# Optimization experiments

Hardware: AMD Instinct MI355X
Metric: run time of the kernel (lower is better)

## Reference

```python
import jax, jax.numpy as jnp
import numpy as np

NUM_HEADS = 16


def setup_inputs() -> dict:
    key = jax.random.key(0)
    ks = jax.random.split(key, 5)
    b, s, d = 2, 2048, 1024
    std = (2.0 / (d + d)) ** 0.5
    x = jax.random.normal(ks[0], (b, s, d), dtype=jnp.float32)
    Wq = jax.random.normal(ks[1], (d, d), dtype=jnp.float32) * std
    Wk = jax.random.normal(ks[2], (d, d), dtype=jnp.float32) * std
    Wv = jax.random.normal(ks[3], (d, d), dtype=jnp.float32) * std
    Wo = jax.random.normal(ks[4], (d, d), dtype=jnp.float32) * std
    return {"x": x, "Wq": Wq, "Wk": Wk, "Wv": Wv, "Wo": Wo}


def reference(x, Wq, Wk, Wv, Wo):
    b, s, d = x.shape
    h = NUM_HEADS
    dk = d // h
    # projections: bias-free x @ W (W is [in, out])
    def split_heads(t):
        return t.reshape(b, s, h, dk).transpose(0, 2, 1, 3)  # b h s dk
    q = split_heads(x @ Wq)
    k = split_heads(x @ Wk)
    v = split_heads(x @ Wv)
    scale = 1.0 / jnp.sqrt(jnp.asarray(dk, dtype=x.dtype))
    scores = jnp.einsum('bhqd,bhkd->bhqk', q, k) * scale  # b h s s
    causal = jnp.tril(jnp.ones((s, s), dtype=bool))
    scores = jnp.where(causal, scores, -jnp.inf)
    probs = jax.nn.softmax(scores, axis=-1)
    out = jnp.einsum('bhqk,bhkd->bhqd', probs, v)
    out = out.transpose(0, 2, 1, 3).reshape(b, s, d)  # b s (h dk)
    return out @ Wo
```

## Files before the change

kernel.cpp:

```cpp
#include <hip/hip_runtime.h>

typedef unsigned short u16;
typedef unsigned int   u32;

using bf16x8 = __attribute__((ext_vector_type(8))) __bf16;
using f32x4  = __attribute__((ext_vector_type(4))) float;
using s16x4  = __attribute__((ext_vector_type(4))) short;

#define NH    16
#define DKH   64
#define SEQ   2048
#define BAT   2
#define DMOD  1024

#define QSCALE 0.18033688011112042f

__device__ __forceinline__ u16 f2bf(float f) {
  union { float f; u32 u; } v; v.f = f;
  u32 r = v.u + 0x7fffu + ((v.u >> 16) & 1u);
  return (u16)(r >> 16);
}

__device__ __forceinline__ u32 pack2bf(float a, float b) {
  union { float f; u32 u; } x, y; x.f = a; y.f = b;
  u32 ua = x.u + 0x7fffu + ((x.u >> 16) & 1u);
  u32 ub = y.u + 0x7fffu + ((y.u >> 16) & 1u);
  return __builtin_amdgcn_perm(ub, ua, 0x07060302u);
}

__device__ __forceinline__ void gll16(const u16* g, u16* l) {
  __builtin_amdgcn_global_load_lds((__attribute__((address_space(1))) void*)(u16*)g,
                                   (__attribute__((address_space(3))) void*)l,
                                   16, 0, 0);
}

#if __has_builtin(__builtin_amdgcn_exp2f)
#define EXP2(x) __builtin_amdgcn_exp2f(x)
#else
#define EXP2(x) exp2f(x)
#endif

#if __has_builtin(__builtin_amdgcn_mfma_f32_16x16x16bf16_1k)
__device__ __forceinline__ f32x4 mfma16(s16x4 a, s16x4 b, f32x4 c) {
  return __builtin_amdgcn_mfma_f32_16x16x16bf16_1k(a, b, c, 0, 0, 0);
}
#else
__device__ __forceinline__ f32x4 mfma16(s16x4 a, s16x4 b, f32x4 c) {
  f32x4 d;
  asm volatile("v_mfma_f32_16x16x16_bf16 %0, %1, %2, %3\n\ts_nop 7\n\ts_nop 7"
               : "=v"(d) : "v"(a), "v"(b), "v"(c));
  return d;
}
#endif

__global__ __launch_bounds__(256) void transpose_all(const float* __restrict__ Wq,
                                                     const float* __restrict__ Wk,
                                                     const float* __restrict__ Wv,
                                                     const float* __restrict__ Wo,
                                                     u16* __restrict__ Wt) {
  __shared__ u16 t[32][33];
  const float* W = blockIdx.z == 0 ? Wq : blockIdx.z == 1 ? Wk : blockIdx.z == 2 ? Wv : Wo;
  u16* o = Wt + (size_t)blockIdx.z * DMOD * DMOD;
  int bx = blockIdx.x * 32, by = blockIdx.y * 32;
  int x = threadIdx.x, y = threadIdx.y;
  #pragma unroll
  for (int i = 0; i < 32; i += 8)
    t[y + i][x] = f2bf(W[(size_t)(by + y + i) * DMOD + bx + x]);
  __syncthreads();
  #pragma unroll
  for (int i = 0; i < 32; i += 8)
    o[(size_t)(bx + y + i) * DMOD + by + x] = t[x][y + i];
}

__global__ __launch_bounds__(256) void convert_x(const float* __restrict__ x,
                                                 u16* __restrict__ xb) {
  size_t i = ((size_t)blockIdx.x * 256 + threadIdx.x) * 8;
  float4 f0 = *(const float4*)(x + i);
  float4 f1 = *(const float4*)(x + i + 4);
  uint4 o;
  o.x = pack2bf(f0.x, f0.y); o.y = pack2bf(f0.z, f0.w);
  o.z = pack2bf(f1.x, f1.y); o.w = pack2bf(f1.z, f1.w);
  *(uint4*)(xb + i) = o;
}

__global__ __launch_bounds__(256) void gemm_qkv(const u16* __restrict__ A,
                                                const u16* __restrict__ Bt,
                                                u16* __restrict__ Qo,
                                                u16* __restrict__ Ko,
                                                u16* __restrict__ Vo) {
  __shared__ __align__(16) u16 As[128 * 64];
  __shared__ __align__(16) u16 Bs[128 * 64];
  const int tid  = threadIdx.x;
  const int lane = tid & 63, wv = tid >> 6;
  const int wm   = wv >> 1, wn = wv & 1;
  const int lrow = lane & 15, quad = lane >> 4;
  const int sw   = lrow & 7;
  const int tileM = blockIdx.x * 128, tileN = blockIdx.y * 128;
  const int srow8 = lane >> 3;
  const int scc   = ((lane & 7) ^ srow8) * 8;

  const f32x4 fz = {0.f, 0.f, 0.f, 0.f};
  f32x4 acc[4][4];
  #pragma unroll
  for (int i = 0; i < 4; ++i)
    #pragma unroll
    for (int j = 0; j < 4; ++j) acc[i][j] = fz;

  for (int kt = 0; kt < DMOD; kt += 64) {
    #pragma unroll
    for (int i = 0; i < 4; ++i) {
      int rb = wv * 32 + i * 8;
      gll16(&A [(size_t)(tileM + rb + srow8) * DMOD + kt + scc], &As[rb * 64]);
      gll16(&Bt[(size_t)(tileN + rb + srow8) * DMOD + kt + scc], &Bs[rb * 64]);
    }
    __syncthreads();
    #pragma unroll
    for (int kk = 0; kk < 2; ++kk) {
      bf16x8 af[4], bfr[4];
      #pragma unroll
      for (int mt = 0; mt < 4; ++mt)
        af[mt] = *(const bf16x8*)(&As[(wm * 64 + mt * 16 + lrow) * 64 +
                                      (((kk * 4 + quad) ^ sw) * 8)]);
      #pragma unroll
      for (int nt = 0; nt < 4; ++nt)
        bfr[nt] = *(const bf16x8*)(&Bs[(wn * 64 + nt * 16 + lrow) * 64 +
                                       (((kk * 4 + quad) ^ sw) * 8)]);
      #pragma unroll
      for (int mt = 0; mt < 4; ++mt)
        #pragma unroll
        for (int nt = 0; nt < 4; ++nt)
          acc[mt][nt] = __builtin_amdgcn_mfma_f32_16x16x32_bf16(af[mt], bfr[nt],
                                                                acc[mt][nt], 0, 0, 0);
    }
    __syncthreads();
  }

  #pragma unroll
  for (int mt = 0; mt < 4; ++mt) {
    #pragma unroll
    for (int nt = 0; nt < 4; ++nt) {
      int gm0 = tileM + wm * 64 + mt * 16 + quad * 4;
      int gn  = tileN + wn * 64 + nt * 16 + lrow;
      int which = gn >> 10, col = gn & 1023;
      int bb = gm0 >> 11, srw0 = gm0 & (SEQ - 1);
      int hh = col >> 6, dki = col & (DKH - 1);
      size_t bhi = (size_t)(bb * NH + hh);
      if (which == 0) {
        #pragma unroll
        for (int r = 0; r < 4; ++r)
          Qo[(bhi * SEQ + srw0 + r) * DKH + dki] = f2bf(acc[mt][nt][r] * QSCALE);
      } else if (which == 1) {
        #pragma unroll
        for (int r = 0; r < 4; ++r)
          Ko[(bhi * SEQ + srw0 + r) * DKH + dki] = f2bf(acc[mt][nt][r]);
      } else {
        uint2 pk;
        pk.x = pack2bf(acc[mt][nt][0], acc[mt][nt][1]);
        pk.y = pack2bf(acc[mt][nt][2], acc[mt][nt][3]);
        *(uint2*)(&Vo[(((bhi * (SEQ / 4)) + (srw0 >> 2)) * DKH + dki) * 4]) = pk;
      }
    }
  }
}

__global__ __launch_bounds__(256) void gemm_out(const u16* __restrict__ A,
                                                const u16* __restrict__ Bt,
                                                float* __restrict__ Co) {
  __shared__ __align__(16) u16 As[128 * 64];
  __shared__ __align__(16) u16 Bs[64 * 64];
  const int tid  = threadIdx.x;
  const int lane = tid & 63, wv = tid >> 6;
  const int wm   = wv & 1, wn = wv >> 1;
  const int lrow = lane & 15, quad = lane >> 4;
  const int sw   = lrow & 7;
  const int tileM = blockIdx.x * 128, tileN = blockIdx.y * 64;
  const int srow8 = lane >> 3;
  const int scc   = ((lane & 7) ^ srow8) * 8;

  const f32x4 fz = {0.f, 0.f, 0.f, 0.f};
  f32x4 acc[4][2];
  #pragma unroll
  for (int i = 0; i < 4; ++i) { acc[i][0] = fz; acc[i][1] = fz; }

  for (int kt = 0; kt < DMOD; kt += 64) {
    #pragma unroll
    for (int i = 0; i < 4; ++i) {
      int rb = wv * 32 + i * 8;
      gll16(&A[(size_t)(tileM + rb + srow8) * DMOD + kt + scc], &As[rb * 64]);
    }
    #pragma unroll
    for (int i = 0; i < 2; ++i) {
      int rb = wv * 16 + i * 8;
      gll16(&Bt[(size_t)(tileN + rb + srow8) * DMOD + kt + scc], &Bs[rb * 64]);
    }
    __syncthreads();
    #pragma unroll
    for (int kk = 0; kk < 2; ++kk) {
      bf16x8 af[4], bfr[2];
      #pragma unroll
      for (int mt = 0; mt < 4; ++mt)
        af[mt] = *(const bf16x8*)(&As[(wm * 64 + mt * 16 + lrow) * 64 +
                                      (((kk * 4 + quad) ^ sw) * 8)]);
      #pragma unroll
      for (int nt = 0; nt < 2; ++nt)
        bfr[nt] = *(const bf16x8*)(&Bs[(wn * 32 + nt * 16 + lrow) * 64 +
                                       (((kk * 4 + quad) ^ sw) * 8)]);
      #pragma unroll
      for (int mt = 0; mt < 4; ++mt)
        #pragma unroll
        for (int nt = 0; nt < 2; ++nt)
          acc[mt][nt] = __builtin_amdgcn_mfma_f32_16x16x32_bf16(af[mt], bfr[nt],
                                                                acc[mt][nt], 0, 0, 0);
    }
    __syncthreads();
  }

  #pragma unroll
  for (int mt = 0; mt < 4; ++mt)
    #pragma unroll
    for (int nt = 0; nt < 2; ++nt)
      #pragma unroll
      for (int r = 0; r < 4; ++r) {
        int gm = tileM + wm * 64 + mt * 16 + quad * 4 + r;
        int gn = tileN + wn * 32 + nt * 16 + lrow;
        Co[(size_t)gm * DMOD + gn] = acc[mt][nt][r];
      }
}

#define KP 72
#define VP 132
#define OP 72

__global__ __launch_bounds__(512) void attn_k(const u16* __restrict__ Q,
                                              const u16* __restrict__ Kg,
                                              const u16* __restrict__ Vg,
                                              u16* __restrict__ Og) {
  __shared__ __align__(16) u16 KsA[128 * KP];
  __shared__ __align__(16) u16 VsA[64 * VP];
  __shared__ __align__(16) u16 KsB[128 * KP];
  __shared__ __align__(16) u16 VsB[64 * VP];
  __shared__ __align__(16) u16 Os[128 * OP];

  const int tid  = threadIdx.x;
  const int lane = tid & 63, w = tid >> 6;
  const int lrow = lane & 15, quad = lane >> 4;
  const int bh = blockIdx.x, pr = blockIdx.y;
  const int b = bh >> 4, h = bh & 15;

  const u16* Qbh = Q  + (size_t)bh * SEQ * DKH;
  const u16* Kbh = Kg + (size_t)bh * SEQ * DKH;
  const u16* Vbh = Vg + (size_t)bh * SEQ * DKH;

  uint4 kreg[2], vreg[2];
  #pragma unroll
  for (int k = 0; k < 2; ++k) {
    int ci = k * 512 + tid;
    kreg[k] = *(const uint4*)(&Kbh[(size_t)(ci >> 3) * DKH + (ci & 7) * 8]);
    vreg[k] = *(const uint4*)(&Vbh[(size_t)(ci >> 5) * 256 + (ci & 31) * 8]);
  }

  int cur = 0;
  const f32x4 fz = {0.f, 0.f, 0.f, 0.f};

  for (int half = 0; half < 2; ++half) {
    const int qt = half ? (15 - pr) : pr;
    const int jmax = qt;
    const int qglob = qt * 128 + w * 16 + lrow;

    bf16x8 bq[2];
    #pragma unroll
    for (int kk = 0; kk < 2; ++kk)
      bq[kk] = *(const bf16x8*)(&Qbh[(size_t)qglob * DKH + kk * 32 + quad * 8]);

    f32x4 oacc[4];
    #pragma unroll
    for (int d = 0; d < 4; ++d) oacc[d] = fz;
    float lsum = 0.f;

    for (int j = 0; j <= jmax; ++j) {
      u16* Ks = cur ? KsB : KsA;
      u16* Vs = cur ? VsB : VsA;

      #pragma unroll
      for (int k = 0; k < 2; ++k) {
        int ci = k * 512 + tid;
        *(uint4*)(&Ks[(ci >> 3) * KP + (ci & 7) * 8]) = kreg[k];
        int sq = ci >> 5, dkp = ci & 31;
        union { uint4 q; uint2 d[2]; } vv; vv.q = vreg[k];
        *(uint2*)(&Vs[(2 * dkp)     * VP + 4 * sq]) = vv.d[0];
        *(uint2*)(&Vs[(2 * dkp + 1) * VP + 4 * sq]) = vv.d[1];
      }

      const bool pf = (j < jmax) || (half == 0);
      if (pf) {
        const int jn = (j < jmax) ? (j + 1) : 0;
        #pragma unroll
        for (int k = 0; k < 2; ++k) {
          int ci = k * 512 + tid;
          kreg[k] = *(const uint4*)(&Kbh[(size_t)(jn * 128 + (ci >> 3)) * DKH + (ci & 7) * 8]);
          vreg[k] = *(const uint4*)(&Vbh[(size_t)(jn * 32 + (ci >> 5)) * 256 + (ci & 31) * 8]);
        }
      }

      __syncthreads();

      if (j < jmax) {
        f32x4 sacc[8];
        #pragma unroll
        for (int m = 0; m < 8; ++m) sacc[m] = fz;
        #pragma unroll
        for (int kk = 0; kk < 2; ++kk)
          #pragma unroll
          for (int m = 0; m < 8; ++m) {
            bf16x8 ak = *(const bf16x8*)(&Ks[(m * 16 + lrow) * KP + kk * 32 + quad * 8]);
            sacc[m] = __builtin_amdgcn_mfma_f32_16x16x32_bf16(ak, bq[kk], sacc[m], 0, 0, 0);
          }
        #pragma unroll
        for (int m = 0; m < 8; ++m)
          #pragma unroll
          for (int r = 0; r < 4; ++r) {
            float p = EXP2(sacc[m][r]);
            sacc[m][r] = p;
            lsum += p;
          }
        #pragma unroll
        for (int m = 0; m < 8; ++m) {
          union { u32 u[2]; s16x4 v; } pk;
          pk.u[0] = pack2bf(sacc[m][0], sacc[m][1]);
          pk.u[1] = pack2bf(sacc[m][2], sacc[m][3]);
          #pragma unroll
          for (int d = 0; d < 4; ++d) {
            s16x4 av = *(const s16x4*)(&Vs[(d * 16 + lrow) * VP + m * 16 + quad * 4]);
            oacc[d] = mfma16(av, pk.v, oacc[d]);
          }
        }
      } else {
        for (int m = 0; m < w; ++m) {
          f32x4 s = fz;
          #pragma unroll
          for (int kk = 0; kk < 2; ++kk) {
            bf16x8 ak = *(const bf16x8*)(&Ks[(m * 16 + lrow) * KP + kk * 32 + quad * 8]);
            s = __builtin_amdgcn_mfma_f32_16x16x32_bf16(ak, bq[kk], s, 0, 0, 0);
          }
          union { u32 u[2]; s16x4 v; } pk;
          float p0 = EXP2(s[0]), p1 = EXP2(s[1]), p2 = EXP2(s[2]), p3 = EXP2(s[3]);
          lsum += (p0 + p1) + (p2 + p3);
          pk.u[0] = pack2bf(p0, p1);
          pk.u[1] = pack2bf(p2, p3);
          #pragma unroll
          for (int d = 0; d < 4; ++d) {
            s16x4 av = *(const s16x4*)(&Vs[(d * 16 + lrow) * VP + m * 16 + quad * 4]);
            oacc[d] = mfma16(av, pk.v, oacc[d]);
          }
        }
        {
          f32x4 s = fz;
          #pragma unroll
          for (int kk = 0; kk < 2; ++kk) {
            bf16x8 ak = *(const bf16x8*)(&Ks[(w * 16 + lrow) * KP + kk * 32 + quad * 8]);
            s = __builtin_amdgcn_mfma_f32_16x16x32_bf16(ak, bq[kk], s, 0, 0, 0);
          }
          float p[4];
          #pragma unroll
          for (int r = 0; r < 4; ++r) {
            int kg = jmax * 128 + w * 16 + quad * 4 + r;
            p[r] = (kg > qglob) ? 0.f : EXP2(s[r]);
            lsum += p[r];
          }
          union { u32 u[2]; s16x4 v; } pk;
          pk.u[0] = pack2bf(p[0], p[1]);
          pk.u[1] = pack2bf(p[2], p[3]);
          #pragma unroll
          for (int d = 0; d < 4; ++d) {
            s16x4 av = *(const s16x4*)(&Vs[(d * 16 + lrow) * VP + w * 16 + quad * 4]);
            oacc[d] = mfma16(av, pk.v, oacc[d]);
          }
        }
      }
      cur ^= 1;
    }

    float ls = lsum;
    ls += __shfl_xor(ls, 16, 64);
    ls += __shfl_xor(ls, 32, 64);
    float inv = 1.f / ls;

    #pragma unroll
    for (int d = 0; d < 4; ++d) {
      uint2 pk;
      pk.x = pack2bf(oacc[d][0] * inv, oacc[d][1] * inv);
      pk.y = pack2bf(oacc[d][2] * inv, oacc[d][3] * inv);
      *(uint2*)(&Os[(w * 16 + lrow) * OP + d * 16 + quad * 4]) = pk;
    }
    __syncthreads();
    #pragma unroll
    for (int k = 0; k < 2; ++k) {
      int c = k * 512 + tid;
      int row = c >> 3, ch = c & 7;
      uint4 v = *(const uint4*)(&Os[row * OP + ch * 8]);
      *(uint4*)(&Og[(size_t)(b * SEQ + qt * 128 + row) * DMOD + h * DKH + ch * 8]) = v;
    }
    __syncthreads();
  }
}

extern "C" void kernel_launch(void* const* d_in, const int* in_sizes, int n_in,
                              void* d_out, int out_size, void* d_ws, size_t ws_size,
                              hipStream_t stream) {
  const float* x  = (const float*)d_in[0];
  const float* Wq = (const float*)d_in[1];
  const float* Wk = (const float*)d_in[2];
  const float* Wv = (const float*)d_in[3];
  const float* Wo = (const float*)d_in[4];

  u16* ws = (u16*)d_ws;
  const size_t WSZ = (size_t)DMOD * DMOD;
  const size_t TSZ = (size_t)BAT * NH * SEQ * DKH;
  u16* Wt  = ws;
  u16* Wto = Wt + 3 * WSZ;
  u16* xb  = Wt + 4 * WSZ;
  u16* Qb  = xb + TSZ;
  u16* Kb  = Qb + TSZ;
  u16* Vb  = Kb + TSZ;
  u16* Ob  = xb;

  transpose_all<<<dim3(32, 32, 4), dim3(32, 8), 0, stream>>>(Wq, Wk, Wv, Wo, Wt);
  convert_x<<<dim3(2048), 256, 0, stream>>>(x, xb);

  gemm_qkv<<<dim3(32, 24), 256, 0, stream>>>(xb, Wt, Qb, Kb, Vb);

  attn_k<<<dim3(32, 8), 512, 0, stream>>>(Qb, Kb, Vb, Ob);

  gemm_out<<<dim3(32, 16), 256, 0, stream>>>(Ob, Wto, (float*)d_out);
}
```

Baseline: 191.3 us.

## Split attention KV range across two blocks and add combine kernel

Replaces the paired-query-tile attention schedule with a split-KV scheme. Each (batch-head, query-tile) now gets two blocks, each covering half of the causal key range and writing unnormalized fp32 partial outputs and row sums. A new combine kernel then adds the partials, normalizes, and writes bf16. This raises the block count from 256 to 1024 so more CUs stay busy, and it drops LDS double buffering. The cost is extra fp32 partial traffic, one more kernel launch, and no overlap of shared-memory stores with compute.

Result: slower. 207.2 us (+8.3%).

```diff
diff --git a/kernel.cpp b/kernel.cpp
--- a/kernel.cpp
+++ b/kernel.cpp
@@ -229,179 +229,184 @@
 
 #define KP 72
 #define VP 132
-#define OP 72
-
-__global__ __launch_bounds__(512) void attn_k(const u16* __restrict__ Q,
-                                              const u16* __restrict__ Kg,
-                                              const u16* __restrict__ Vg,
-                                              u16* __restrict__ Og) {
-  __shared__ __align__(16) u16 KsA[128 * KP];
-  __shared__ __align__(16) u16 VsA[64 * VP];
-  __shared__ __align__(16) u16 KsB[128 * KP];
-  __shared__ __align__(16) u16 VsB[64 * VP];
-  __shared__ __align__(16) u16 Os[128 * OP];
+
+__global__ __launch_bounds__(512, 4) void attn_k(const u16* __restrict__ Q,
+                                                 const u16* __restrict__ Kg,
+                                                 const u16* __restrict__ Vg,
+                                                 float* __restrict__ Opart,
+                                                 float* __restrict__ lpart) {
+  __shared__ __align__(16) u16 Ks[128 * KP];
+  __shared__ __align__(16) u16 Vs[64 * VP];
 
   const int tid  = threadIdx.x;
   const int lane = tid & 63, w = tid >> 6;
   const int lrow = lane & 15, quad = lane >> 4;
-  const int bh = blockIdx.x, pr = blockIdx.y;
-  const int b = bh >> 4, h = bh & 15;
+  const int bh = blockIdx.x, qt = blockIdx.y, s = blockIdx.z;
+  const int split = (qt + 2) >> 1;
+  const int j0 = s ? split : 0;
+  const int j1 = s ? (qt + 1) : split;
+
+  const int p = s * 512 + bh * 16 + qt;
+  float* Op = Opart + (size_t)p * (128 * 64);
+
+  if (j0 >= j1) {
+    const f32x4 fz = {0.f, 0.f, 0.f, 0.f};
+    for (int t = tid; t < 128 * 64 / 4; t += 512) ((f32x4*)Op)[t] = fz;
+    if (tid < 128) lpart[(size_t)p * 128 + tid] = 0.f;
+    return;
+  }
 
   const u16* Qbh = Q  + (size_t)bh * SEQ * DKH;
   const u16* Kbh = Kg + (size_t)bh * SEQ * DKH;
   const u16* Vbh = Vg + (size_t)bh * SEQ * DKH;
 
+  const int qglob = qt * 128 + w * 16 + lrow;
+  bf16x8 bq[2];
+  #pragma unroll
+  for (int kk = 0; kk < 2; ++kk)
+    bq[kk] = *(const bf16x8*)(&Qbh[(size_t)qglob * DKH + kk * 32 + quad * 8]);
+
   uint4 kreg[2], vreg[2];
   #pragma unroll
   for (int k = 0; k < 2; ++k) {
     int ci = k * 512 + tid;
-    kreg[k] = *(const uint4*)(&Kbh[(size_t)(ci >> 3) * DKH + (ci & 7) * 8]);
-    vreg[k] = *(const uint4*)(&Vbh[(size_t)(ci >> 5) * 256 + (ci & 31) * 8]);
-  }
-
-  int cur = 0;
+    kreg[k] = *(const uint4*)(&Kbh[(size_t)(j0 * 128 + (ci >> 3)) * DKH + (ci & 7) * 8]);
+    vreg[k] = *(const uint4*)(&Vbh[(size_t)(j0 * 32 + (ci >> 5)) * 256 + (ci & 31) * 8]);
+  }
+
   const f32x4 fz = {0.f, 0.f, 0.f, 0.f};
-
-  for (int half = 0; half < 2; ++half) {
-    const int qt = half ? (15 - pr) : pr;
-    const int jmax = qt;
-    const int qglob = qt * 128 + w * 16 + lrow;
-
-    bf16x8 bq[2];
-    #pragma unroll
-    for (int kk = 0; kk < 2; ++kk)
-      bq[kk] = *(const bf16x8*)(&Qbh[(size_t)qglob * DKH + kk * 32 + quad * 8]);
-
-    f32x4 oacc[4];
-    #pragma unroll
-    for (int d = 0; d < 4; ++d) oacc[d] = fz;
-    float lsum = 0.f;
-
-    for (int j = 0; j <= jmax; ++j) {
-      u16* Ks = cur ? KsB : KsA;
-      u16* Vs = cur ? VsB : VsA;
-
+  f32x4 oacc[4];
+  #pragma unroll
+  for (int d = 0; d < 4; ++d) oacc[d] = fz;
+  float lsum = 0.f;
+
+  for (int j = j0; j < j1; ++j) {
+    __syncthreads();
+    #pragma unroll
+    for (int k = 0; k < 2; ++k) {
+      int ci = k * 512 + tid;
+      *(uint4*)(&Ks[(ci >> 3) * KP + (ci & 7) * 8]) = kreg[k];
+      int sq = ci >> 5, dkp = ci & 31;
+      union { uint4 q; uint2 d[2]; } vv; vv.q = vreg[k];
+      *(uint2*)(&Vs[(2 * dkp)     * VP + 4 * sq]) = vv.d[0];
+      *(uint2*)(&Vs[(2 * dkp + 1) * VP + 4 * sq]) = vv.d[1];
+    }
+    if (j + 1 < j1) {
       #pragma unroll
       for (int k = 0; k < 2; ++k) {
         int ci = k * 512 + tid;
-        *(uint4*)(&Ks[(ci >> 3) * KP + (ci & 7) * 8]) = kreg[k];
-        int sq = ci >> 5, dkp = ci & 31;
-        union { uint4 q; uint2 d[2]; } vv; vv.q = vreg[k];
-        *(uint2*)(&Vs[(2 * dkp)     * VP + 4 * sq]) = vv.d[0];
-        *(uint2*)(&Vs[(2 * dkp + 1) * VP + 4 * sq]) = vv.d[1];
-      }
-
-      const bool pf = (j < jmax) || (half == 0);
-      if (pf) {
-        const int jn = (j < jmax) ? (j + 1) : 0;
-        #pragma unroll
-        for (int k = 0; k < 2; ++k) {
-          int ci = k * 512 + tid;
-          kreg[k] = *(const uint4*)(&Kbh[(size_t)(jn * 128 + (ci >> 3)) * DKH + (ci & 7) * 8]);
-          vreg[k] = *(const uint4*)(&Vbh[(size_t)(jn * 32 + (ci >> 5)) * 256 + (ci & 31) * 8]);
-        }
-      }
-
-      __syncthreads();
-
-      if (j < jmax) {
-        f32x4 sacc[8];
-        #pragma unroll
-        for (int m = 0; m < 8; ++m) sacc[m] = fz;
-        #pragma unroll
-        for (int kk = 0; kk < 2; ++kk)
-          #pragma unroll
-          for (int m = 0; m < 8; ++m) {
-            bf16x8 ak = *(const bf16x8*)(&Ks[(m * 16 + lrow) * KP + kk * 32 + quad * 8]);
-            sacc[m] = __builtin_amdgcn_mfma_f32_16x16x32_bf16(ak, bq[kk], sacc[m], 0, 0, 0);
-          }
-        #pragma unroll
-        for (int m = 0; m < 8; ++m)
-          #pragma unroll
-          for (int r = 0; r < 4; ++r) {
-            float p = EXP2(sacc[m][r]);
-            sacc[m][r] = p;
-            lsum += p;
-          }
+        kreg[k] = *(const uint4*)(&Kbh[(size_t)((j + 1) * 128 + (ci >> 3)) * DKH + (ci & 7) * 8]);
+        vreg[k] = *(const uint4*)(&Vbh[(size_t)((j + 1) * 32 + (ci >> 5)) * 256 + (ci & 31) * 8]);
+      }
+    }
+    __syncthreads();
+
+    if (j < qt) {
+      f32x4 sacc[8];
+      #pragma unroll
+      for (int m = 0; m < 8; ++m) sacc[m] = fz;
+      #pragma unroll
+      for (int kk = 0; kk < 2; ++kk)
         #pragma unroll
         for (int m = 0; m < 8; ++m) {
-          union { u32 u[2]; s16x4 v; } pk;
-          pk.u[0] = pack2bf(sacc[m][0], sacc[m][1]);
-          pk.u[1] = pack2bf(sacc[m][2], sacc[m][3]);
-          #pragma unroll
-          for (int d = 0; d < 4; ++d) {
-            s16x4 av = *(const s16x4*)(&Vs[(d * 16 + lrow) * VP + m * 16 + quad * 4]);
-            oacc[d] = mfma16(av, pk.v, oacc[d]);
-          }
-        }
-      } else {
-        for (int m = 0; m < w; ++m) {
-          f32x4 s = fz;
-          #pragma unroll
-          for (int kk = 0; kk < 2; ++kk) {
-            bf16x8 ak = *(const bf16x8*)(&Ks[(m * 16 + lrow) * KP + kk * 32 + quad * 8]);
-            s = __builtin_amdgcn_mfma_f32_16x16x32_bf16(ak, bq[kk], s, 0, 0, 0);
-          }
-          union { u32 u[2]; s16x4 v; } pk;
-          float p0 = EXP2(s[0]), p1 = EXP2(s[1]), p2 = EXP2(s[2]), p3 = EXP2(s[3]);
-          lsum += (p0 + p1) + (p2 + p3);
-          pk.u[0] = pack2bf(p0, p1);
-          pk.u[1] = pack2bf(p2, p3);
-          #pragma unroll
-          for (int d = 0; d < 4; ++d) {
-            s16x4 av = *(const s16x4*)(&Vs[(d * 16 + lrow) * VP + m * 16 + quad * 4]);
-            oacc[d] = mfma16(av, pk.v, oacc[d]);
-          }
-        }
-        {
-          f32x4 s = fz;
-          #pragma unroll
-          for (int kk = 0; kk < 2; ++kk) {
-            bf16x8 ak = *(const bf16x8*)(&Ks[(w * 16 + lrow) * KP + kk * 32 + quad * 8]);
-            s = __builtin_amdgcn_mfma_f32_16x16x32_bf16(ak, bq[kk], s, 0, 0, 0);
-          }
-          float p[4];
-          #pragma unroll
-          for (int r = 0; r < 4; ++r) {
-            int kg = jmax * 128 + w * 16 + quad * 4 + r;
-            p[r] = (kg > qglob) ? 0.f : EXP2(s[r]);
-            lsum += p[r];
-          }
-          union { u32 u[2]; s16x4 v; } pk;
-          pk.u[0] = pack2bf(p[0], p[1]);
-          pk.u[1] = pack2bf(p[2], p[3]);
-          #pragma unroll
-          for (int d = 0; d < 4; ++d) {
-            s16x4 av = *(const s16x4*)(&Vs[(d * 16 + lrow) * VP + w * 16 + quad * 4]);
-            oacc[d] = mfma16(av, pk.v, oacc[d]);
-          }
-        }
-      }
-      cur ^= 1;
-    }
-
-    float ls = lsum;
-    ls += __shfl_xor(ls, 16, 64);
-    ls += __shfl_xor(ls, 32, 64);
-    float inv = 1.f / ls;
-
-    #pragma unroll
-    for (int d = 0; d < 4; ++d) {
-      uint2 pk;
-      pk.x = pack2bf(oacc[d][0] * inv, oacc[d][1] * inv);
-      pk.y = pack2bf(oacc[d][2] * inv, oacc[d][3] * inv);
-      *(uint2*)(&Os[(w * 16 + lrow) * OP + d * 16 + quad * 4]) = pk;
-    }
-    __syncthreads();
-    #pragma unroll
-    for (int k = 0; k < 2; ++k) {
-      int c = k * 512 + tid;
-      int row = c >> 3, ch = c & 7;
-      uint4 v = *(const uint4*)(&Os[row * OP + ch * 8]);
-      *(uint4*)(&Og[(size_t)(b * SEQ + qt * 128 + row) * DMOD + h * DKH + ch * 8]) = v;
-    }
-    __syncthreads();
-  }
+          bf16x8 ak = *(const bf16x8*)(&Ks[(m * 16 + lrow) * KP + kk * 32 + quad * 8]);
+          sacc[m] = __builtin_amdgcn_mfma_f32_16x16x32_bf16(ak, bq[kk], sacc[m], 0, 0, 0);
+        }
+      #pragma unroll
+      for (int m = 0; m < 8; ++m)
+        #pragma unroll
+        for (int r = 0; r < 4; ++r) {
+          float pv = EXP2(sacc[m][r]);
+          sacc[m][r] = pv;
+          lsum += pv;
+        }
+      #pragma unroll
+      for (int m = 0; m < 8; ++m) {
+        union { u32 u[2]; s16x4 v; } pk;
+        pk.u[0] = pack2bf(sacc[m][0], sacc[m][1]);
+        pk.u[1] = pack2bf(sacc[m][2], sacc[m][3]);
+        #pragma unroll
+        for (int d = 0; d < 4; ++d) {
+          s16x4 av = *(const s16x4*)(&Vs[(d * 16 + lrow) * VP + m * 16 + quad * 4]);
+          oacc[d] = mfma16(av, pk.v, oacc[d]);
+        }
+      }
+    } else {
+      for (int m = 0; m < w; ++m) {
+        f32x4 sv = fz;
+        #pragma unroll
+        for (int kk = 0; kk < 2; ++kk) {
+          bf16x8 ak = *(const bf16x8*)(&Ks[(m * 16 + lrow) * KP + kk * 32 + quad * 8]);
+          sv = __builtin_amdgcn_mfma_f32_16x16x32_bf16(ak, bq[kk], sv, 0, 0, 0);
+        }
+        union { u32 u[2]; s16x4 v; } pk;
+        float p0 = EXP2(sv[0]), p1 = EXP2(sv[1]), p2 = EXP2(sv[2]), p3 = EXP2(sv[3]);
+        lsum += (p0 + p1) + (p2 + p3);
+        pk.u[0] = pack2bf(p0, p1);
+        pk.u[1] = pack2bf(p2, p3);
+        #pragma unroll
+        for (int d = 0; d < 4; ++d) {
+          s16x4 av = *(const s16x4*)(&Vs[(d * 16 + lrow) * VP + m * 16 + quad * 4]);
+          oacc[d] = mfma16(av, pk.v, oacc[d]);
+        }
+      }
+      {
+        f32x4 sv = fz;
+        #pragma unroll
+        for (int kk = 0; kk < 2; ++kk) {
+          bf16x8 ak = *(const bf16x8*)(&Ks[(w * 16 + lrow) * KP + kk * 32 + quad * 8]);
+          sv = __builtin_amdgcn_mfma_f32_16x16x32_bf16(ak, bq[kk], sv, 0, 0, 0);
+        }
+        float pv[4];
+        #pragma unroll
+        for (int r = 0; r < 4; ++r) {
+          int kg = qt * 128 + w * 16 + quad * 4 + r;
+          pv[r] = (kg > qglob) ? 0.f : EXP2(sv[r]);
+          lsum += pv[r];
+        }
+        union { u32 u[2]; s16x4 v; } pk;
+        pk.u[0] = pack2bf(pv[0], pv[1]);
+        pk.u[1] = pack2bf(pv[2], pv[3]);
+        #pragma unroll
+        for (int d = 0; d < 4; ++d) {
+          s16x4 av = *(const s16x4*)(&Vs[(d * 16 + lrow) * VP + w * 16 + quad * 4]);
+          oacc[d] = mfma16(av, pk.v, oacc[d]);
+        }
+      }
+    }
+  }
+
+  float ls = lsum;
+  ls += __shfl_xor(ls, 16, 64);
+  ls += __shfl_xor(ls, 32, 64);
+  if (quad == 0) lpart[(size_t)p * 128 + w * 16 + lrow] = ls;
+
+  const int row = w * 16 + lrow;
+  #pragma unroll
+  for (int d = 0; d < 4; ++d)
+    *(f32x4*)(&Op[(size_t)row * 64 + d * 16 + quad * 4]) = oacc[d];
+}
+
+__global__ __launch_bounds__(256) void combine_k(const float* __restrict__ Opart,
+                                                 const float* __restrict__ lpart,
+                                                 u16* __restrict__ Ob) {
+  int t = blockIdx.x * 256 + threadIdx.x;
+  int dk4 = t & 15;
+  int row = (t >> 4) & 127;
+  int qt  = (t >> 11) & 15;
+  int bh  = t >> 15;
+  size_t prow0 = ((size_t)(bh * 16 + qt)) * 128 + row;
+  size_t prow1 = prow0 + 512 * 128;
+  f32x4 a = *(const f32x4*)(&Opart[prow0 * 64 + dk4 * 4]);
+  f32x4 b = *(const f32x4*)(&Opart[prow1 * 64 + dk4 * 4]);
+  float inv = 1.f / (lpart[prow0] + lpart[prow1]);
+  f32x4 c = (a + b) * inv;
+  int bb = bh >> 4, h = bh & 15;
+  int srow = qt * 128 + row;
+  uint2 pk;
+  pk.x = pack2bf(c[0], c[1]);
+  pk.y = pack2bf(c[2], c[3]);
+  *(uint2*)(&Ob[((size_t)(bb * SEQ + srow)) * DMOD + h * DKH + dk4 * 4]) = pk;
 }
 
 extern "C" void kernel_launch(void* const* d_in, const int* in_sizes, int n_in,
@@ -423,13 +428,16 @@
   u16* Kb  = Qb + TSZ;
   u16* Vb  = Kb + TSZ;
   u16* Ob  = xb;
+  float* Opart = (float*)(Vb + TSZ);
+  float* lpart = Opart + (size_t)1024 * 128 * 64;
 
   transpose_all<<<dim3(32, 32, 4), dim3(32, 8), 0, stream>>>(Wq, Wk, Wv, Wo, Wt);
   convert_x<<<dim3(2048), 256, 0, stream>>>(x, xb);
 
   gemm_qkv<<<dim3(32, 24), 256, 0, stream>>>(xb, Wt, Qb, Kb, Vb);
 
-  attn_k<<<dim3(32, 8), 512, 0, stream>>>(Qb, Kb, Vb, Ob);
+  attn_k<<<dim3(32, 16, 2), 512, 0, stream>>>(Qb, Kb, Vb, Opart, lpart);
+  combine_k<<<dim3(4096), 256, 0, stream>>>(Opart, lpart, Ob);
 
   gemm_out<<<dim3(32, 16), 256, 0, stream>>>(Ob, Wto, (float*)d_out);
 }
```
